# Optimization experiments

Hardware: AMD Instinct MI355X
Metric: run time of the kernel (lower is better)

The kernel has to match this reference:

```python
import jax, jax.numpy as jnp
import numpy as np

# ---- config (matches init_kwargs) ----
GROUP_NUM = 2048
K_NEIGHBORS = 32
OUT_DIM = 192
SIGMA, BASELINE, SCALING, EPS = 0.26, 0.1, 10.0, 1e-6
ALPHA, BETA = 1000.0, 100.0
ADAPTIVE_RATIO = 0.5
IN_DIM = 3
ADAPTIVE_DIM = int(OUT_DIM * ADAPTIVE_RATIO)          # 96
FOURIER_DIM = OUT_DIM - ADAPTIVE_DIM                  # 96
FEAT_DIM_F = FOURIER_DIM // (IN_DIM * 2)              # 16
FEAT_DIM_A = int(np.ceil(ADAPTIVE_DIM / IN_DIM))      # 32
FEAT_NUM_A = FEAT_DIM_A * IN_DIM                      # 96
OUT_IDX = np.linspace(0, FEAT_NUM_A - 1, ADAPTIVE_DIM).astype(np.int64)


def setup_inputs() -> dict:
    key = jax.random.key(0)
    k1, k2, k3, k4 = jax.random.split(key, 4)
    xyz = jax.random.normal(k1, (4, 8192, 3), dtype=jnp.float32)
    x = jax.random.normal(k2, (4, 8192, 96), dtype=jnp.float32)
    bn_gamma = jax.random.uniform(k3, (192,), dtype=jnp.float32)
    bn_beta = jax.random.normal(k4, (192,), dtype=jnp.float32)
    return {"xyz": xyz, "x": x, "bn_gamma": bn_gamma, "bn_beta": bn_beta}


def _fps(xyz, m):
    """Farthest point sampling. xyz: [B,N,3] -> idx [B,m] (int32). Seed = index 0."""
    def single(pts):
        n = pts.shape[0]
        def step(carry, _):
            dists, last = carry
            d = jnp.sum((pts - pts[last]) ** 2, axis=-1)
            dists = jnp.minimum(dists, d)
            nxt = jnp.argmax(dists).astype(jnp.int32)
            return (dists, nxt), nxt
        init = (jnp.full((n,), 1e10, pts.dtype), jnp.array(0, jnp.int32))
        _, idxs = jax.lax.scan(step, init, None, length=m - 1)
        return jnp.concatenate([jnp.zeros((1,), jnp.int32), idxs])
    return jax.vmap(single)(xyz)


def _square_distance(src, dst):
    # src: [B,S,3], dst: [B,N,3] -> [B,S,N]
    d = -2.0 * jnp.einsum('bsc,bnc->bsn', src, dst)
    d += jnp.sum(src ** 2, -1)[:, :, None]
    d += jnp.sum(dst ** 2, -1)[:, None, :]
    return d


def _gather_knn(points, idx):
    # points: [B,N,C], idx: [B,G,K] -> [B,G,K,C]
    return jax.vmap(lambda p, i: p[i])(points, idx)


def _forward(xyz, x, bn_gamma, bn_beta):
    B, N, _ = xyz.shape
    G, K = GROUP_NUM, K_NEIGHBORS

    # ---- Grouper_seg ----
    fps_idx = _fps(xyz, G)                                   # [B,G]
    lc_xyz = jnp.take_along_axis(xyz, fps_idx[..., None], 1)  # [B,G,3]
    lc_x = jnp.take_along_axis(x, fps_idx[..., None], 1)      # [B,G,C]
    sqr = _square_distance(lc_xyz, xyz)                       # [B,G,N]
    knn_idx = jax.lax.top_k(-sqr, K)[1]                       # [B,G,K] smallest-k
    knn_xyz = _gather_knn(xyz, knn_idx)                       # [B,G,K,3]
    knn_x = _gather_knn(x, knn_idx)                           # [B,G,K,C]

    # ---- Aggregation_seg: local normalization ----
    mean_x = lc_x[:, :, None, :]
    std_x = jnp.std(knn_x - mean_x, ddof=1)
    mean_xyz = lc_xyz[:, :, None, :]
    std_xyz = jnp.std(knn_xyz - mean_xyz, ddof=1)
    knn_x = (knn_x - mean_x) / (std_x + 1e-5)
    knn_xyz_n = (knn_xyz - mean_xyz) / (std_xyz + 1e-5)       # [B,G,K,3]
    C = knn_x.shape[-1]
    knn_x = jnp.concatenate(
        [knn_x, jnp.broadcast_to(lc_x[:, :, None, :], (B, G, K, C))], axis=-1)  # [B,G,K,2C]
    knn_xyz_cf = jnp.transpose(knn_xyz_n, (0, 3, 1, 2))       # [B,3,G,K]
    knn_x_cf = jnp.transpose(knn_x, (0, 3, 1, 2))             # [B,OUT_DIM,G,K]

    # ---- PosE_Geo: fourier part ----
    feat_range = jnp.arange(FEAT_DIM_F, dtype=knn_xyz_cf.dtype)
    dim_embed = ALPHA ** (feat_range / FEAT_DIM_F)            # [F]
    div = BETA * knn_xyz_cf[..., None] / dim_embed            # [B,3,G,K,F]
    fourier = jnp.stack([jnp.sin(div), jnp.cos(div)], axis=-1)  # [B,3,G,K,F,2]
    fourier = fourier.reshape(B, IN_DIM, G, K, 2 * FEAT_DIM_F)
    fourier = jnp.transpose(fourier, (0, 1, 4, 2, 3)).reshape(B, FOURIER_DIM, G, K)

    # ---- AdaptiveEmbedding (parameterless, data-driven) ----
    x4 = knn_xyz_n                                            # [B,G,K,3]
    gstd = jnp.mean(jnp.std(x4.reshape(B, -1, IN_DIM), axis=1, ddof=1))
    sig = SIGMA * (1.0 + gstd) + EPS
    blend = jax.nn.sigmoid((gstd - BASELINE) * SCALING)
    feat_val = jnp.linspace(-1.0, 1.0, FEAT_DIM_A + 2)[1:-1]  # [Fa]
    z = (x4[..., None] - feat_val) / sig                      # [B,G,K,3,Fa]
    comb = blend * jnp.exp(-0.5 * z * z) + (1.0 - blend) * jnp.cos(z)
    ae = comb.reshape(B, G, K, FEAT_NUM_A)[..., OUT_IDX]      # [B,G,K,ADAPTIVE_DIM]
    ae_cf = jnp.transpose(ae, (0, 3, 1, 2))                   # [B,ADAPTIVE_DIM,G,K]

    pe = jnp.concatenate([fourier, ae_cf], axis=1)            # [B,OUT_DIM,G,K]
    knn_x_w = (knn_x_cf + pe) * pe

    # ---- Pooling_seg: max+mean pool, BatchNorm1d (train stats) + GELU ----
    lc = jnp.max(knn_x_w, -1) + jnp.mean(knn_x_w, -1)         # [B,OUT_DIM,G]
    mu = jnp.mean(lc, axis=(0, 2), keepdims=True)
    var = jnp.var(lc, axis=(0, 2), keepdims=True)
    y = (lc - mu) / jnp.sqrt(var + 1e-5)
    y = y * bn_gamma[None, :, None] + bn_beta[None, :, None]
    return jax.nn.gelu(y, approximate=False)


def reference(xyz, x, bn_gamma, bn_beta):
    return _forward(xyz, x, bn_gamma, bn_beta)
```

## Files before the change

kernel.cpp:

```cpp
#include <hip/hip_runtime.h>
#include <cstdint>
#include <math.h>

#define NPTS 8192
#define NB 4
#define NG 2048
#define NK 32
#define CIN 96
#define COUT 192

typedef unsigned long long ull;

__global__ __launch_bounds__(256) void setup_kernel(const float* __restrict__ xyz,
                                                    float* __restrict__ xs, float* __restrict__ ys,
                                                    float* __restrict__ zs, float* __restrict__ d2){
  int i = blockIdx.x*256 + threadIdx.x;
  if (i >= NB*NPTS) return;
  float x = xyz[3*i+0], y = xyz[3*i+1], z = xyz[3*i+2];
  xs[i]=x; ys[i]=y; zs[i]=z;
  d2[i] = __fadd_rn(__fadd_rn(__fmul_rn(x,x),__fmul_rn(y,y)),__fmul_rn(z,z));
}

template<int CTRL>
__device__ __forceinline__ void dppmax_pair(unsigned& hi, unsigned& lo){
  unsigned ohi = (unsigned)__builtin_amdgcn_update_dpp((int)hi, (int)hi, CTRL, 0xf, 0xf, false);
  unsigned olo = (unsigned)__builtin_amdgcn_update_dpp((int)lo, (int)lo, CTRL, 0xf, 0xf, false);
  bool gt = (ohi > hi) || (ohi == hi && olo > lo);
  hi = gt ? ohi : hi;
  lo = gt ? olo : lo;
}

__global__ __launch_bounds__(1024,4) void fps_kernel(const float* __restrict__ xyz, int* __restrict__ fps_idx){
#pragma clang fp contract(off)
  extern __shared__ char smem[];
  float4* ctab = (float4*)smem;
  ull*    keys = (ull*)(smem + 131072);
  int*    hist = (int*)(smem + 131072 + 256);
  float*  bbs  = (float*)(smem + 131072 + 256 + 2048);
  const int b = blockIdx.x, t = threadIdx.x;
  const int w = t>>6, lane = t&63;
  const float* base = xyz + (size_t)b*NPTS*3;

  float ox[8], oy[8], oz[8];
#pragma unroll
  for (int j=0;j<8;++j){
    int p = t + 1024*j;
    ox[j]=base[3*p+0]; oy[j]=base[3*p+1]; oz[j]=base[3*p+2];
  }
  float mnx=ox[0],mxx=ox[0],mny=oy[0],mxy=oy[0],mnz=oz[0],mxz=oz[0];
#pragma unroll
  for (int j=1;j<8;++j){
    mnx=fminf(mnx,ox[j]); mxx=fmaxf(mxx,ox[j]);
    mny=fminf(mny,oy[j]); mxy=fmaxf(mxy,oy[j]);
    mnz=fminf(mnz,oz[j]); mxz=fmaxf(mxz,oz[j]);
  }
#pragma unroll
  for (int off=32; off>0; off>>=1){
    mnx=fminf(mnx,__shfl_xor(mnx,off)); mxx=fmaxf(mxx,__shfl_xor(mxx,off));
    mny=fminf(mny,__shfl_xor(mny,off)); mxy=fmaxf(mxy,__shfl_xor(mxy,off));
    mnz=fminf(mnz,__shfl_xor(mnz,off)); mxz=fmaxf(mxz,__shfl_xor(mxz,off));
  }
  if (t < 512) hist[t] = 0;
  if (lane==0){
    bbs[w*6+0]=mnx; bbs[w*6+1]=mxx; bbs[w*6+2]=mny;
    bbs[w*6+3]=mxy; bbs[w*6+4]=mnz; bbs[w*6+5]=mxz;
  }
  if (t==0) fps_idx[b*NG] = 0;
  __syncthreads();
  float gx0=1e30f,gx1=-1e30f,gy0=1e30f,gy1=-1e30f,gz0=1e30f,gz1=-1e30f;
  for (int q=0;q<16;++q){
    gx0=fminf(gx0,bbs[q*6+0]); gx1=fmaxf(gx1,bbs[q*6+1]);
    gy0=fminf(gy0,bbs[q*6+2]); gy1=fmaxf(gy1,bbs[q*6+3]);
    gz0=fminf(gz0,bbs[q*6+4]); gz1=fmaxf(gz1,bbs[q*6+5]);
  }
  const float sxv = 8.0f/fmaxf(gx1-gx0,1e-20f);
  const float syv = 8.0f/fmaxf(gy1-gy0,1e-20f);
  const float szv = 8.0f/fmaxf(gz1-gz0,1e-20f);
  int cell[8];
#pragma unroll
  for (int j=0;j<8;++j){
    int cx = min(7,(int)((ox[j]-gx0)*sxv));
    int cy = min(7,(int)((oy[j]-gy0)*syv));
    int cz = min(7,(int)((oz[j]-gz0)*szv));
    int m = (cx&1) | ((cy&1)<<1) | ((cz&1)<<2)
          | ((cx&2)<<2) | ((cy&2)<<3) | ((cz&2)<<4)
          | ((cx&4)<<4) | ((cy&4)<<5) | ((cz&4)<<6);
    cell[j]=m;
    atomicAdd(&hist[m],1);
  }
  __syncthreads();
  if (t < 64){
    int s0[8];
#pragma unroll
    for (int j=0;j<8;++j) s0[j]=hist[t*8+j];
    int tot=0;
#pragma unroll
    for (int j=0;j<8;++j){ int v=s0[j]; s0[j]=tot; tot+=v; }
    int inc=tot;
#pragma unroll
    for (int off=1; off<64; off<<=1){
      int o=__shfl_up(inc,off);
      if (t>=off) inc+=o;
    }
    int excl=inc-tot;
#pragma unroll
    for (int j=0;j<8;++j) hist[t*8+j]=excl+s0[j];
  }
  __syncthreads();
#pragma unroll
  for (int j=0;j<8;++j){
    int pos = atomicAdd(&hist[cell[j]],1);
    ctab[pos] = make_float4(ox[j],oy[j],oz[j], __int_as_float(t+1024*j));
  }
  __syncthreads();
  float px[8],py[8],pz[8],D[8]; unsigned lowb[8];
  float bx0,bx1,by0,by1,bz0,bz1;
#pragma unroll
  for (int j=0;j<8;++j){
    int pos = (w<<9) + (j<<6) + lane;
    float4 c4 = ctab[pos];
    px[j]=c4.x; py[j]=c4.y; pz[j]=c4.z;
    unsigned orig = (unsigned)__float_as_int(c4.w);
    lowb[j] = ((8191u-orig)<<13) | (unsigned)pos;
    D[j] = 1e10f;
    asm volatile("" : "+v"(px[j]), "+v"(py[j]), "+v"(pz[j]), "+v"(lowb[j]));
    if (j==0){ bx0=px[j]; bx1=px[j]; by0=py[j]; by1=py[j]; bz0=pz[j]; bz1=pz[j]; }
    else {
      bx0=fminf(bx0,px[j]); bx1=fmaxf(bx1,px[j]);
      by0=fminf(by0,py[j]); by1=fmaxf(by1,py[j]);
      bz0=fminf(bz0,pz[j]); bz1=fmaxf(bz1,pz[j]);
    }
  }
#pragma unroll
  for (int off=32; off>0; off>>=1){
    bx0=fminf(bx0,__shfl_xor(bx0,off)); bx1=fmaxf(bx1,__shfl_xor(bx1,off));
    by0=fminf(by0,__shfl_xor(by0,off)); by1=fmaxf(by1,__shfl_xor(by1,off));
    bz0=fminf(bz0,__shfl_xor(bz0,off)); bz1=fmaxf(bz1,__shfl_xor(bz1,off));
  }

  float lx=base[0], ly=base[1], lz=base[2];
  float Mw = 1e10f;
  unsigned mylow = 0;
  for (int it=0; it<NG-1; ++it){
    float qx=fminf(fmaxf(lx,bx0),bx1);
    float qy=fminf(fmaxf(ly,by0),by1);
    float qz=fminf(fmaxf(lz,bz0),bz1);
    float ddx=qx-lx, ddy=qy-ly, ddz=qz-lz;
    float LB = (ddx*ddx+ddy*ddy)+ddz*ddz;
    ull* kslot = &keys[(it&1)*16 + w];
    if (LB <= Mw*1.0001f){
      float bd=-1.0f;
#pragma unroll
      for (int j=0;j<8;++j){
        float dx=px[j]-lx, dy=py[j]-ly, dz=pz[j]-lz;
        float d=(dx*dx+dy*dy)+dz*dz;
        float nd=fminf(D[j],d);
        D[j]=nd;
        bd=fmaxf(bd,nd);
      }
      unsigned bl=0;
#pragma unroll
      for (int j=0;j<8;++j){
        unsigned c2 = (lowb[j]>bl)?lowb[j]:bl;
        bl = (D[j]==bd) ? c2 : bl;
      }
      unsigned hi = __float_as_uint(bd), lo = bl;
      dppmax_pair<0x111>(hi,lo); dppmax_pair<0x112>(hi,lo); dppmax_pair<0x114>(hi,lo);
      dppmax_pair<0x118>(hi,lo); dppmax_pair<0x142>(hi,lo); dppmax_pair<0x143>(hi,lo);
      unsigned hw  = (unsigned)__builtin_amdgcn_readlane((int)hi,63);
      unsigned lwv = (unsigned)__builtin_amdgcn_readlane((int)lo,63);
      if (lane==63) *kslot = (((ull)hw)<<32) | (ull)lwv;
      Mw = __uint_as_float(hw);
      mylow = lwv;
    } else {
      if (lane==63) *kslot = (((ull)__float_as_uint(Mw))<<32) | (ull)mylow;
    }
    __syncthreads();
    const ull* kk = keys + (it&1)*16;
    ull k = kk[0];
#pragma unroll
    for (int q=1;q<16;++q){ ull o=kk[q]; if (o>k) k=o; }
    unsigned lw = (unsigned)k;
    float4 c4 = ctab[lw & 0x1FFFu];
    lx=c4.x; ly=c4.y; lz=c4.z;
    if (t==0) fps_idx[b*NG + it + 1] = (int)(8191u - ((lw>>13)&0x1FFFu));
  }
}

__device__ __forceinline__ bool lexlt(float ad, int ai, float bd, int bi){
  return (ad < bd) || ((ad == bd) && (ai < bi));
}
__device__ __forceinline__ void sort_desc(float& d, int& i, int lane){
#pragma unroll
  for (int k=2;k<=64;k<<=1){
#pragma unroll
    for (int j=k>>1;j>0;j>>=1){
      float od = __shfl_xor(d, j);
      int   oi = __shfl_xor(i, j);
      bool dirUp = (lane & k) != 0;
      bool lower = (lane & j) == 0;
      bool less  = lexlt(d,i,od,oi);
      bool keep  = (less == (lower == dirUp));
      if (!keep){ d=od; i=oi; }
    }
  }
}
__device__ __forceinline__ void merge_asc(float& d, int& i, int lane){
#pragma unroll
  for (int j=32;j>0;j>>=1){
    float od = __shfl_xor(d, j);
    int   oi = __shfl_xor(i, j);
    bool lower = (lane & j) == 0;
    bool less  = lexlt(d,i,od,oi);
    bool keep  = (less == lower);
    if (!keep){ d=od; i=oi; }
  }
}

__global__ __launch_bounds__(256) void knn_kernel(const float* __restrict__ xs, const float* __restrict__ ys,
                                                  const float* __restrict__ zs, const float* __restrict__ d2,
                                                  const int* __restrict__ fps_idx, int* __restrict__ knn_out){
  __shared__ float tx[256], ty[256], tz[256], td[256];
  const int tid = threadIdx.x;
  const int wid = tid>>6, lane = tid&63;
  const int pid = blockIdx.x*4 + wid;
  const int b = pid >> 11;
  const float* bx = xs + b*NPTS;
  const float* by = ys + b*NPTS;
  const float* bz = zs + b*NPTS;
  const float* bD = d2 + b*NPTS;
  const int fi = fps_idx[pid];
  const float ax = bx[fi], ay = by[fi], az = bz[fi];
  const float src2 = __fadd_rn(__fadd_rn(__fmul_rn(ax,ax),__fmul_rn(ay,ay)),__fmul_rn(az,az));
  float Ad = INFINITY; int Ai = 0x7fffffff;
  float tau_d = INFINITY; int tau_i = 0x7fffffff;
  for (int s=0; s<NPTS/256; ++s){
    __syncthreads();
    int gidx = s*256 + tid;
    tx[tid]=bx[gidx]; ty[tid]=by[gidx]; tz[tid]=bz[gidx]; td[tid]=bD[gidx];
    __syncthreads();
    float m0,m1,m2,m3; int i0,i1,i2,i3;
#define LOADJ(mj, ij, J) { int li = (J)*64 + lane; \
    float dot = __fadd_rn(__fadd_rn(__fmul_rn(ax,tx[li]),__fmul_rn(ay,ty[li])),__fmul_rn(az,tz[li])); \
    mj = __fadd_rn(__fadd_rn(__fmul_rn(-2.0f,dot), src2), td[li]); ij = s*256 + li; }
    LOADJ(m0,i0,0) LOADJ(m1,i1,1) LOADJ(m2,i2,2) LOADJ(m3,i3,3)
#undef LOADJ
    while (true){
      bool any = lexlt(m0,i0,tau_d,tau_i) || lexlt(m1,i1,tau_d,tau_i) ||
                 lexlt(m2,i2,tau_d,tau_i) || lexlt(m3,i3,tau_d,tau_i);
      if (__ballot(any) == 0ull) break;
      float cd = m0; int ci = i0; int sel = 0;
      if (lexlt(m1,i1,cd,ci)){ cd=m1; ci=i1; sel=1; }
      if (lexlt(m2,i2,cd,ci)){ cd=m2; ci=i2; sel=2; }
      if (lexlt(m3,i3,cd,ci)){ cd=m3; ci=i3; sel=3; }
      if      (sel==0) m0=INFINITY;
      else if (sel==1) m1=INFINITY;
      else if (sel==2) m2=INFINITY;
      else             m3=INFINITY;
      sort_desc(cd, ci, lane);
      if (lexlt(cd,ci,Ad,Ai)){ Ad=cd; Ai=ci; }
      merge_asc(Ad, Ai, lane);
      tau_d = __shfl(Ad, 31);
      tau_i = __shfl(Ai, 31);
    }
  }
  if (lane < NK) knn_out[pid*NK + lane] = Ai;
}

__global__ __launch_bounds__(256) void stats_kernel(const float* __restrict__ x, const float* __restrict__ xyz,
                                                    const int* __restrict__ fps_idx, const int* __restrict__ knn,
                                                    double* __restrict__ partials){
  const int tid=threadIdx.x, wid=tid>>6, lane=tid&63;
  const int pid = blockIdx.x*4 + wid;
  const int b = pid>>11;
  const int fi = fps_idx[pid];
  const float* xb = x + (size_t)b*NPTS*CIN;
  const float* zb = xyz + (size_t)b*NPTS*3;
  const float lc0 = xb[fi*CIN + lane];
  float lc1 = 0.f; if (lane<32) lc1 = xb[fi*CIN + 64 + lane];
  float czv = 0.f; if (lane<3)  czv = zb[fi*3 + lane];
  double s1=0.0, s2=0.0, a1=0.0, a2=0.0;
  for (int k=0;k<NK;++k){
    int idx = knn[pid*NK + k];
    float d0 = __fsub_rn(xb[idx*CIN + lane], lc0);
    s1 += (double)d0; s2 += (double)d0*(double)d0;
    if (lane<32){
      float d1 = __fsub_rn(xb[idx*CIN + 64 + lane], lc1);
      s1 += (double)d1; s2 += (double)d1*(double)d1;
    }
    if (lane<3){
      float w = __fsub_rn(zb[idx*3 + lane], czv);
      a1 += (double)w; a2 += (double)w*(double)w;
    }
  }
#pragma unroll
  for (int off=32; off>0; off>>=1){ s1 += __shfl_xor(s1,off); s2 += __shfl_xor(s2,off); }
  __shared__ double shx[4][2];
  __shared__ double shz[4][3][2];
  if (lane==0){ shx[wid][0]=s1; shx[wid][1]=s2; }
  if (lane<3){ shz[wid][lane][0]=a1; shz[wid][lane][1]=a2; }
  __syncthreads();
  if (tid==0){
    double u0=0,u1=0;
    for (int w=0;w<4;++w){ u0+=shx[w][0]; u1+=shx[w][1]; }
    double* outp = partials + (size_t)blockIdx.x*8;
    outp[0]=u0; outp[1]=u1;
    for (int axq=0; axq<3; ++axq){
      double v0=0,v1=0;
      for (int w=0;w<4;++w){ v0+=shz[w][axq][0]; v1+=shz[w][axq][1]; }
      outp[2+2*axq]=v0; outp[3+2*axq]=v1;
    }
  }
}

__global__ void finalize_kernel(const double* __restrict__ partials, float* __restrict__ scal){
  const int lane = threadIdx.x;
  double s1=0,s2=0;
  double z0a=0,z0b=0,z1a=0,z1b=0,z2a=0,z2b=0;
  for (int i=0;i<32;++i){
    const double* p = partials + (size_t)(lane*32+i)*8;
    s1+=p[0]; s2+=p[1];
    z0a+=p[2]; z0b+=p[3]; z1a+=p[4]; z1b+=p[5]; z2a+=p[6]; z2b+=p[7];
  }
#pragma unroll
  for (int off=32; off>0; off>>=1){ s1+=__shfl_xor(s1,off); s2+=__shfl_xor(s2,off); }
#pragma unroll
  for (int off=8; off>0; off>>=1){
    z0a+=__shfl_xor(z0a,off); z0b+=__shfl_xor(z0b,off);
    z1a+=__shfl_xor(z1a,off); z1b+=__shfl_xor(z1b,off);
    z2a+=__shfl_xor(z2a,off); z2b+=__shfl_xor(z2b,off);
  }
  __shared__ double zb[4][3][2];
  if ((lane&15)==0){
    int b = lane>>4;
    zb[b][0][0]=z0a; zb[b][0][1]=z0b;
    zb[b][1][0]=z1a; zb[b][1][1]=z1b;
    zb[b][2][0]=z2a; zb[b][2][1]=z2b;
  }
  __syncthreads();
  if (lane==0){
    double nx = (double)NB*NG*NK*CIN;
    double varx = (s2 - s1*s1/nx)/(nx-1.0);
    float stdx = (float)sqrt(varx);
    double t1=0,t2=0;
    for (int b=0;b<4;++b) for (int a=0;a<3;++a){ t1+=zb[b][a][0]; t2+=zb[b][a][1]; }
    double nz = (double)NB*NG*NK*3;
    double varz = (t2 - t1*t1/nz)/(nz-1.0);
    float stdz = (float)sqrt(varz);
    float sdiv = stdz + 1e-5f;
    double n2 = (double)NG*NK;
    double acc=0.0;
    for (int b=0;b<4;++b) for (int a=0;a<3;++a){
      double v = (zb[b][a][1] - zb[b][a][0]*zb[b][a][0]/n2)/(n2-1.0);
      acc += sqrt(v);
    }
    float gstd = (float)(acc/12.0) / sdiv;
    float sig = 0.26f*(1.0f+gstd) + 1e-6f;
    float blend = 1.0f/(1.0f + expf(-(gstd-0.1f)*10.0f));
    scal[0] = 1.0f/(stdx + 1e-5f);
    scal[1] = 1.0f/sdiv;
    scal[2] = 1.0f/sig;
    scal[3] = blend;
  }
}

__global__ __launch_bounds__(256) void main_kernel(const float* __restrict__ x, const float* __restrict__ xyz,
                                                   const int* __restrict__ fps_idx, const int* __restrict__ knn,
                                                   const float* __restrict__ scal, float* __restrict__ lc_out){
  const int tid=threadIdx.x, wid=tid>>6, lane=tid&63;
  const int pid = blockIdx.x*4 + wid;
  const int b = pid>>11, g = pid&2047;
  const float inv_x = scal[0], inv_z = scal[1], inv_sig = scal[2], blend = scal[3];
  const float omb = 1.0f - blend;
  const int fi = fps_idx[pid];
  const float* xb = x + (size_t)b*NPTS*CIN;
  const float* zb = xyz + (size_t)b*NPTS*3;
  const float cx = zb[fi*3+0], cy = zb[fi*3+1], cz = zb[fi*3+2];
  const float lcx0 = xb[fi*CIN + lane];
  const float lcx1 = (lane<32) ? xb[fi*CIN + 64 + lane] : xb[fi*CIN + lane - 32];
  const float lcx2 = xb[fi*CIN + 32 + lane];
  const int dim0 = lane>>5;
  const int rr0 = lane&31;
  const bool cos0 = rr0 & 1;
  const float bs0 = 100.0f / powf(1000.0f, (float)(rr0>>1) * (1.0f/16.0f));
  const bool cos1 = lane & 1;
  const float bs1 = 100.0f / powf(1000.0f, (float)((lane&31)>>1) * (1.0f/16.0f));
  const float fv1 = (float)(-1.0 + 2.0*(double)(lane-32+1)/33.0);
  const int dim2 = (32+lane)>>5;
  const int j2 = (32+lane)&31;
  const float fv2 = (float)(-1.0 + 2.0*(double)(j2+1)/33.0);

  float mx0=-INFINITY, mx1=-INFINITY, mx2=-INFINITY;
  float sm0=0.f, sm1=0.f, sm2=0.f;
  for (int k=0;k<NK;++k){
    const int idx = knn[pid*NK + k];
    const float p0 = zb[idx*3+0], p1 = zb[idx*3+1], p2v = zb[idx*3+2];
    const float xn0 = (p0-cx)*inv_z, xn1 = (p1-cy)*inv_z, xn2 = (p2v-cz)*inv_z;
    const float xk0 = xb[idx*CIN + lane];
    float xk1 = 0.f; if (lane<32) xk1 = xb[idx*CIN + 64 + lane];
    {
      float v = dim0 ? xn1 : xn0;
      float a = v * bs0;
      float pe = cos0 ? __cosf(a) : __sinf(a);
      float f = (xk0 - lcx0) * inv_x;
      float w = (f + pe) * pe;
      mx0 = fmaxf(mx0, w); sm0 += w;
    }
    {
      float pe, f;
      if (lane < 32){
        float a = xn2 * bs1;
        pe = cos1 ? __cosf(a) : __sinf(a);
        f = (xk1 - lcx1) * inv_x;
      } else {
        float zq = (xn0 - fv1) * inv_sig;
        pe = blend * __expf(-0.5f*zq*zq) + omb * __cosf(zq);
        f = lcx1;
      }
      float w = (f + pe) * pe;
      mx1 = fmaxf(mx1, w); sm1 += w;
    }
    {
      float v = (dim2==1) ? xn1 : xn2;
      float zq = (v - fv2) * inv_sig;
      float pe = blend * __expf(-0.5f*zq*zq) + omb * __cosf(zq);
      float w = (lcx2 + pe) * pe;
      mx2 = fmaxf(mx2, w); sm2 += w;
    }
  }
  const size_t obase = ((size_t)b*COUT)*NG + g;
  lc_out[obase + (size_t)lane*NG]       = mx0 + sm0*(1.0f/32.0f);
  lc_out[obase + (size_t)(64+lane)*NG]  = mx1 + sm1*(1.0f/32.0f);
  lc_out[obase + (size_t)(128+lane)*NG] = mx2 + sm2*(1.0f/32.0f);
}

__global__ __launch_bounds__(256) void bn_stats_kernel(const float* __restrict__ lc, float* __restrict__ bn){
  const int c = blockIdx.x, t = threadIdx.x, lane=t&63, wid=t>>6;
  double s1=0.0, s2=0.0;
  for (int i=t; i<NB*NG; i+=256){
    int b=i>>11, g=i&2047;
    float v = lc[((size_t)(b*COUT)+c)*NG + g];
    s1 += (double)v; s2 += (double)v*(double)v;
  }
#pragma unroll
  for (int off=32; off>0; off>>=1){ s1+=__shfl_xor(s1,off); s2+=__shfl_xor(s2,off); }
  __shared__ double sh1[4], sh2[4];
  if (lane==0){ sh1[wid]=s1; sh2[wid]=s2; }
  __syncthreads();
  if (t==0){
    double a=sh1[0]+sh1[1]+sh1[2]+sh1[3], q=sh2[0]+sh2[1]+sh2[2]+sh2[3];
    double n=(double)(NB*NG);
    double mu=a/n, var=q/n - mu*mu;
    bn[c]=(float)mu;
    bn[COUT+c]=(float)(1.0/sqrt(var + 1e-5));
  }
}

__global__ __launch_bounds__(256) void final_kernel(const float* __restrict__ bn, const float* __restrict__ gamma,
                                                    const float* __restrict__ beta, float* __restrict__ out){
  int i = blockIdx.x*256 + threadIdx.x;
  int c = (i >> 11) % COUT;
  float v = out[i];
  float y = (v - bn[c]) * bn[COUT + c];
  y = y*gamma[c] + beta[c];
  out[i] = y * 0.5f * (1.0f + erff(y * 0.70710678118654752f));
}

extern "C" void kernel_launch(void* const* d_in, const int* in_sizes, int n_in,
                              void* d_out, int out_size, void* d_ws, size_t ws_size,
                              hipStream_t stream){
  const float* xyz   = (const float*)d_in[0];
  const float* x     = (const float*)d_in[1];
  const float* gamma = (const float*)d_in[2];
  const float* beta  = (const float*)d_in[3];
  float* out = (float*)d_out;
  char* ws = (char*)d_ws;
  int*    fps  = (int*)   (ws + 0);
  int*    knn  = (int*)   (ws + 32768);
  float*  xs   = (float*) (ws + 1081344);
  float*  ys   = (float*) (ws + 1212416);
  float*  zs   = (float*) (ws + 1343488);
  float*  d2   = (float*) (ws + 1474560);
  double* parts= (double*)(ws + 1605632);
  float*  scal = (float*) (ws + 1736704);
  float*  bn   = (float*) (ws + 1736768);

  const int fps_lds = 131072 + 256 + 2048 + 384;
  (void)hipFuncSetAttribute(reinterpret_cast<const void*>(fps_kernel),
                            hipFuncAttributeMaxDynamicSharedMemorySize, fps_lds);

  setup_kernel   <<<dim3((NB*NPTS+255)/256), dim3(256), 0, stream>>>(xyz, xs, ys, zs, d2);
  fps_kernel     <<<dim3(NB),                dim3(1024), fps_lds, stream>>>(xyz, fps);
  knn_kernel     <<<dim3(NB*NG/4),           dim3(256), 0, stream>>>(xs, ys, zs, d2, fps, knn);
  stats_kernel   <<<dim3(NB*NG/4),           dim3(256), 0, stream>>>(x, xyz, fps, knn, parts);
  finalize_kernel<<<dim3(1),                 dim3(64),  0, stream>>>(parts, scal);
  main_kernel    <<<dim3(NB*NG/4),           dim3(256), 0, stream>>>(x, xyz, fps, knn, scal, out);
  bn_stats_kernel<<<dim3(COUT),              dim3(256), 0, stream>>>(out, bn);
  final_kernel   <<<dim3((NB*COUT*NG)/256),  dim3(256), 0, stream>>>(bn, gamma, beta, out);
}
```

Baseline: 3.001 ms.

## Halve FPS block to 512 threads with two-level bbox culling and LDS coordinates

```diff
diff --git a/kernel.cpp b/kernel.cpp
--- a/kernel.cpp
+++ b/kernel.cpp
@@ -30,26 +30,39 @@
   lo = gt ? olo : lo;
 }
 
-__global__ __launch_bounds__(1024,4) void fps_kernel(const float* __restrict__ xyz, int* __restrict__ fps_idx){
+__device__ __forceinline__ ull umax64(ull a, ull b){ return (a > b) ? a : b; }
+
+__device__ __forceinline__ float bbox_lb(float lx, float ly, float lz,
+                                         float x0, float x1, float y0, float y1,
+                                         float z0, float z1){
+#pragma clang fp contract(off)
+  float qx = fminf(fmaxf(lx,x0),x1);
+  float qy = fminf(fmaxf(ly,y0),y1);
+  float qz = fminf(fmaxf(lz,z0),z1);
+  float dx = qx-lx, dy = qy-ly, dz = qz-lz;
+  return (dx*dx+dy*dy)+dz*dz;
+}
+
+__global__ __launch_bounds__(512,2) void fps_kernel(const float* __restrict__ xyz, int* __restrict__ fps_idx){
 #pragma clang fp contract(off)
   extern __shared__ char smem[];
   float4* ctab = (float4*)smem;
   ull*    keys = (ull*)(smem + 131072);
-  int*    hist = (int*)(smem + 131072 + 256);
-  float*  bbs  = (float*)(smem + 131072 + 256 + 2048);
+  int*    hist = (int*)(smem + 131072 + 128);
+  float*  bbs  = (float*)(smem + 131072 + 128 + 2048);
   const int b = blockIdx.x, t = threadIdx.x;
   const int w = t>>6, lane = t&63;
   const float* base = xyz + (size_t)b*NPTS*3;
 
-  float ox[8], oy[8], oz[8];
-#pragma unroll
-  for (int j=0;j<8;++j){
-    int p = t + 1024*j;
+  float ox[16], oy[16], oz[16];
+#pragma unroll
+  for (int j=0;j<16;++j){
+    int p = t + 512*j;
     ox[j]=base[3*p+0]; oy[j]=base[3*p+1]; oz[j]=base[3*p+2];
   }
   float mnx=ox[0],mxx=ox[0],mny=oy[0],mxy=oy[0],mnz=oz[0],mxz=oz[0];
 #pragma unroll
-  for (int j=1;j<8;++j){
+  for (int j=1;j<16;++j){
     mnx=fminf(mnx,ox[j]); mxx=fmaxf(mxx,ox[j]);
     mny=fminf(mny,oy[j]); mxy=fmaxf(mxy,oy[j]);
     mnz=fminf(mnz,oz[j]); mxz=fmaxf(mxz,oz[j]);
@@ -60,7 +73,7 @@
     mny=fminf(mny,__shfl_xor(mny,off)); mxy=fmaxf(mxy,__shfl_xor(mxy,off));
     mnz=fminf(mnz,__shfl_xor(mnz,off)); mxz=fmaxf(mxz,__shfl_xor(mxz,off));
   }
-  if (t < 512) hist[t] = 0;
+  hist[t] = 0;
   if (lane==0){
     bbs[w*6+0]=mnx; bbs[w*6+1]=mxx; bbs[w*6+2]=mny;
     bbs[w*6+3]=mxy; bbs[w*6+4]=mnz; bbs[w*6+5]=mxz;
@@ -68,7 +81,7 @@
   if (t==0) fps_idx[b*NG] = 0;
   __syncthreads();
   float gx0=1e30f,gx1=-1e30f,gy0=1e30f,gy1=-1e30f,gz0=1e30f,gz1=-1e30f;
-  for (int q=0;q<16;++q){
+  for (int q=0;q<8;++q){
     gx0=fminf(gx0,bbs[q*6+0]); gx1=fmaxf(gx1,bbs[q*6+1]);
     gy0=fminf(gy0,bbs[q*6+2]); gy1=fmaxf(gy1,bbs[q*6+3]);
     gz0=fminf(gz0,bbs[q*6+4]); gz1=fmaxf(gz1,bbs[q*6+5]);
@@ -76,9 +89,9 @@
   const float sxv = 8.0f/fmaxf(gx1-gx0,1e-20f);
   const float syv = 8.0f/fmaxf(gy1-gy0,1e-20f);
   const float szv = 8.0f/fmaxf(gz1-gz0,1e-20f);
-  int cell[8];
-#pragma unroll
-  for (int j=0;j<8;++j){
+  int cell[16];
+#pragma unroll
+  for (int j=0;j<16;++j){
     int cx = min(7,(int)((ox[j]-gx0)*sxv));
     int cy = min(7,(int)((oy[j]-gy0)*syv));
     int cz = min(7,(int)((oz[j]-gz0)*szv));
@@ -108,59 +121,75 @@
   }
   __syncthreads();
 #pragma unroll
-  for (int j=0;j<8;++j){
+  for (int j=0;j<16;++j){
     int pos = atomicAdd(&hist[cell[j]],1);
-    ctab[pos] = make_float4(ox[j],oy[j],oz[j], __int_as_float(t+1024*j));
-  }
-  __syncthreads();
-  float px[8],py[8],pz[8],D[8]; unsigned lowb[8];
-  float bx0,bx1,by0,by1,bz0,bz1;
-#pragma unroll
-  for (int j=0;j<8;++j){
-    int pos = (w<<9) + (j<<6) + lane;
+    ctab[pos] = make_float4(ox[j],oy[j],oz[j], __int_as_float(t+512*j));
+  }
+  __syncthreads();
+  float D[16]; unsigned lowb[16];
+  float hx0[2],hx1[2],hy0[2],hy1[2],hz0[2],hz1[2];
+#pragma unroll
+  for (int j=0;j<16;++j){
+    int pos = (w<<10) + (j<<6) + lane;
     float4 c4 = ctab[pos];
-    px[j]=c4.x; py[j]=c4.y; pz[j]=c4.z;
     unsigned orig = (unsigned)__float_as_int(c4.w);
     lowb[j] = ((8191u-orig)<<13) | (unsigned)pos;
     D[j] = 1e10f;
-    asm volatile("" : "+v"(px[j]), "+v"(py[j]), "+v"(pz[j]), "+v"(lowb[j]));
-    if (j==0){ bx0=px[j]; bx1=px[j]; by0=py[j]; by1=py[j]; bz0=pz[j]; bz1=pz[j]; }
+    const int h = j>>3;
+    if ((j&7)==0){ hx0[h]=c4.x; hx1[h]=c4.x; hy0[h]=c4.y; hy1[h]=c4.y; hz0[h]=c4.z; hz1[h]=c4.z; }
     else {
-      bx0=fminf(bx0,px[j]); bx1=fmaxf(bx1,px[j]);
-      by0=fminf(by0,py[j]); by1=fmaxf(by1,py[j]);
-      bz0=fminf(bz0,pz[j]); bz1=fmaxf(bz1,pz[j]);
-    }
-  }
-#pragma unroll
-  for (int off=32; off>0; off>>=1){
-    bx0=fminf(bx0,__shfl_xor(bx0,off)); bx1=fmaxf(bx1,__shfl_xor(bx1,off));
-    by0=fminf(by0,__shfl_xor(by0,off)); by1=fmaxf(by1,__shfl_xor(by1,off));
-    bz0=fminf(bz0,__shfl_xor(bz0,off)); bz1=fmaxf(bz1,__shfl_xor(bz1,off));
-  }
+      hx0[h]=fminf(hx0[h],c4.x); hx1[h]=fmaxf(hx1[h],c4.x);
+      hy0[h]=fminf(hy0[h],c4.y); hy1[h]=fmaxf(hy1[h],c4.y);
+      hz0[h]=fminf(hz0[h],c4.z); hz1[h]=fmaxf(hz1[h],c4.z);
+    }
+  }
+#pragma unroll
+  for (int h=0;h<2;++h){
+#pragma unroll
+    for (int off=32; off>0; off>>=1){
+      hx0[h]=fminf(hx0[h],__shfl_xor(hx0[h],off)); hx1[h]=fmaxf(hx1[h],__shfl_xor(hx1[h],off));
+      hy0[h]=fminf(hy0[h],__shfl_xor(hy0[h],off)); hy1[h]=fmaxf(hy1[h],__shfl_xor(hy1[h],off));
+      hz0[h]=fminf(hz0[h],__shfl_xor(hz0[h],off)); hz1[h]=fmaxf(hz1[h],__shfl_xor(hz1[h],off));
+    }
+  }
+  const float bx0=fminf(hx0[0],hx0[1]), bx1=fmaxf(hx1[0],hx1[1]);
+  const float by0=fminf(hy0[0],hy0[1]), by1=fmaxf(hy1[0],hy1[1]);
+  const float bz0=fminf(hz0[0],hz0[1]), bz1=fmaxf(hz1[0],hz1[1]);
 
   float lx=base[0], ly=base[1], lz=base[2];
   float Mw = 1e10f;
   unsigned mylow = 0;
   for (int it=0; it<NG-1; ++it){
-    float qx=fminf(fmaxf(lx,bx0),bx1);
-    float qy=fminf(fmaxf(ly,by0),by1);
-    float qz=fminf(fmaxf(lz,bz0),bz1);
-    float ddx=qx-lx, ddy=qy-ly, ddz=qz-lz;
-    float LB = (ddx*ddx+ddy*ddy)+ddz*ddz;
-    ull* kslot = &keys[(it&1)*16 + w];
-    if (LB <= Mw*1.0001f){
+    const float thr = Mw*1.0001f;
+    float LB = bbox_lb(lx,ly,lz, bx0,bx1,by0,by1,bz0,bz1);
+    ull* kslot = &keys[(it&1)*8 + w];
+    if (LB <= thr){
+      float LB0 = bbox_lb(lx,ly,lz, hx0[0],hx1[0],hy0[0],hy1[0],hz0[0],hz1[0]);
+      float LB1 = bbox_lb(lx,ly,lz, hx0[1],hx1[1],hy0[1],hy1[1],hz0[1],hz1[1]);
+      if (LB0 <= thr){
+#pragma unroll
+        for (int j=0;j<8;++j){
+          float4 c4 = ctab[(w<<10) + (j<<6) + lane];
+          float dx=c4.x-lx, dy=c4.y-ly, dz=c4.z-lz;
+          float d=(dx*dx+dy*dy)+dz*dz;
+          D[j]=fminf(D[j],d);
+        }
+      }
+      if (LB1 <= thr){
+#pragma unroll
+        for (int j=8;j<16;++j){
+          float4 c4 = ctab[(w<<10) + (j<<6) + lane];
+          float dx=c4.x-lx, dy=c4.y-ly, dz=c4.z-lz;
+          float d=(dx*dx+dy*dy)+dz*dz;
+          D[j]=fminf(D[j],d);
+        }
+      }
       float bd=-1.0f;
 #pragma unroll
-      for (int j=0;j<8;++j){
-        float dx=px[j]-lx, dy=py[j]-ly, dz=pz[j]-lz;
-        float d=(dx*dx+dy*dy)+dz*dz;
-        float nd=fminf(D[j],d);
-        D[j]=nd;
-        bd=fmaxf(bd,nd);
-      }
+      for (int j=0;j<16;++j) bd=fmaxf(bd,D[j]);
       unsigned bl=0;
 #pragma unroll
-      for (int j=0;j<8;++j){
+      for (int j=0;j<16;++j){
         unsigned c2 = (lowb[j]>bl)?lowb[j]:bl;
         bl = (D[j]==bd) ? c2 : bl;
       }
@@ -176,10 +205,11 @@
       if (lane==63) *kslot = (((ull)__float_as_uint(Mw))<<32) | (ull)mylow;
     }
     __syncthreads();
-    const ull* kk = keys + (it&1)*16;
-    ull k = kk[0];
-#pragma unroll
-    for (int q=1;q<16;++q){ ull o=kk[q]; if (o>k) k=o; }
+    const ulonglong2* kk2 = (const ulonglong2*)(keys + (it&1)*8);
+    ulonglong2 p0 = kk2[0], p1 = kk2[1], p2 = kk2[2], p3 = kk2[3];
+    ull a0 = umax64(p0.x, p0.y), a1 = umax64(p1.x, p1.y);
+    ull a2 = umax64(p2.x, p2.y), a3 = umax64(p3.x, p3.y);
+    ull k  = umax64(umax64(a0,a1), umax64(a2,a3));
     unsigned lw = (unsigned)k;
     float4 c4 = ctab[lw & 0x1FFFu];
     lx=c4.x; ly=c4.y; lz=c4.z;
@@ -485,12 +515,12 @@
   float*  scal = (float*) (ws + 1736704);
   float*  bn   = (float*) (ws + 1736768);
 
-  const int fps_lds = 131072 + 256 + 2048 + 384;
+  const int fps_lds = 131072 + 128 + 2048 + 192;
   (void)hipFuncSetAttribute(reinterpret_cast<const void*>(fps_kernel),
                             hipFuncAttributeMaxDynamicSharedMemorySize, fps_lds);
 
   setup_kernel   <<<dim3((NB*NPTS+255)/256), dim3(256), 0, stream>>>(xyz, xs, ys, zs, d2);
-  fps_kernel     <<<dim3(NB),                dim3(1024), fps_lds, stream>>>(xyz, fps);
+  fps_kernel     <<<dim3(NB),                dim3(512), fps_lds, stream>>>(xyz, fps);
   knn_kernel     <<<dim3(NB*NG/4),           dim3(256), 0, stream>>>(xs, ys, zs, d2, fps, knn);
   stats_kernel   <<<dim3(NB*NG/4),           dim3(256), 0, stream>>>(x, xyz, fps, knn, parts);
   finalize_kernel<<<dim3(1),                 dim3(64),  0, stream>>>(parts, scal);
```

Result: faster. 2.915 ms (-2.9%).
